# Performance work log

Hardware: AMD Instinct MI355X
Metric: run time of the kernel (lower is better)

Reference implementation:

```python
import jax, jax.numpy as jnp
import numpy as np

DIM = 512
HEADS = 8
D_HEAD = 64
INNER = HEADS * D_HEAD  # 512
CTX_DIM = 768
FF_INNER = 4 * DIM  # 2048
SCALE = D_HEAD ** -0.5
LN_EPS = 1e-5


def layer_norm(x, g, b):
    mu = jnp.mean(x, axis=-1, keepdims=True)
    var = jnp.var(x, axis=-1, keepdims=True)
    return (x - mu) * jax.lax.rsqrt(var + LN_EPS) * g + b


def attention(x, ctx, qw, kw, vw, ow, ob):
    B, N, _ = x.shape
    M = ctx.shape[1]
    q = (x @ qw).reshape(B, N, HEADS, D_HEAD).transpose(0, 2, 1, 3)
    k = (ctx @ kw).reshape(B, M, HEADS, D_HEAD).transpose(0, 2, 1, 3)
    v = (ctx @ vw).reshape(B, M, HEADS, D_HEAD).transpose(0, 2, 1, 3)
    sim = jnp.einsum('bhid,bhjd->bhij', q, k) * SCALE  # [B,H,N,M]
    attn = jax.nn.softmax(sim, axis=-1)
    out = jnp.einsum('bhij,bhjd->bhid', attn, v)
    out = out.transpose(0, 2, 1, 3).reshape(B, N, INNER)
    return out @ ow + ob


def setup_inputs() -> dict:
    key = jax.random.key(0)
    ks = jax.random.split(key, 20)
    r = lambda k, shp, s=0.02: jax.random.normal(k, shp, dtype=jnp.float32) * s
    return {
        'x': jax.random.normal(ks[0], (2, 4096, DIM), dtype=jnp.float32),
        'context': jax.random.normal(ks[1], (2, 256, CTX_DIM), dtype=jnp.float32),
        'q1_w': r(ks[2], (DIM, INNER)), 'k1_w': r(ks[3], (DIM, INNER)),
        'v1_w': r(ks[4], (DIM, INNER)), 'o1_w': r(ks[5], (INNER, DIM)),
        'o1_b': jnp.zeros((DIM,), jnp.float32),
        'q2_w': r(ks[6], (DIM, INNER)), 'k2_w': r(ks[7], (CTX_DIM, INNER)),
        'v2_w': r(ks[8], (CTX_DIM, INNER)), 'o2_w': r(ks[9], (INNER, DIM)),
        'o2_b': jnp.zeros((DIM,), jnp.float32),
        'ff_in_w': r(ks[10], (DIM, 2 * FF_INNER)), 'ff_in_b': jnp.zeros((2 * FF_INNER,), jnp.float32),
        'ff_out_w': r(ks[11], (FF_INNER, DIM)), 'ff_out_b': jnp.zeros((DIM,), jnp.float32),
        'ln1_g': jnp.ones((DIM,), jnp.float32), 'ln1_b': jnp.zeros((DIM,), jnp.float32),
        'ln2_g': jnp.ones((DIM,), jnp.float32), 'ln2_b': jnp.zeros((DIM,), jnp.float32),
        'ln3_g': jnp.ones((DIM,), jnp.float32), 'ln3_b': jnp.zeros((DIM,), jnp.float32),
    }


def reference(x, context, q1_w, k1_w, v1_w, o1_w, o1_b,
              q2_w, k2_w, v2_w, o2_w, o2_b,
              ff_in_w, ff_in_b, ff_out_w, ff_out_b,
              ln1_g, ln1_b, ln2_g, ln2_b, ln3_g, ln3_b):
    # self-attention + residual
    h = layer_norm(x, ln1_g, ln1_b)
    x = attention(h, h, q1_w, k1_w, v1_w, o1_w, o1_b) + x
    # cross-attention + residual
    h = layer_norm(x, ln2_g, ln2_b)
    x = attention(h, context, q2_w, k2_w, v2_w, o2_w, o2_b) + x
    # GEGLU feed-forward + residual (torch F.gelu is exact erf form)
    h = layer_norm(x, ln3_g, ln3_b)
    proj = h @ ff_in_w + ff_in_b
    val, gate = jnp.split(proj, 2, axis=-1)
    ff = (val * jax.nn.gelu(gate, approximate=False)) @ ff_out_w + ff_out_b
    return ff + x
```

## Files before the change

### kernel.cpp

```cpp
#include <hip/hip_runtime.h>
#include <hip/hip_bf16.h>
#include <cstdint>


typedef __bf16 bf16_t;
typedef __bf16 bf16x8 __attribute__((ext_vector_type(8)));
typedef float f32x4 __attribute__((ext_vector_type(4)));
typedef float f32x16 __attribute__((ext_vector_type(16)));

__device__ __forceinline__ bf16_t f2bf(float f) { return (bf16_t)f; }

__device__ __forceinline__ f32x4 mfma16(bf16x8 a, bf16x8 b, f32x4 c) {
  return __builtin_amdgcn_mfma_f32_16x16x32_bf16(a, b, c, 0, 0, 0);
}
__device__ __forceinline__ f32x16 mfma32(bf16x8 a, bf16x8 b, f32x16 c) {
  return __builtin_amdgcn_mfma_f32_32x32x16_bf16(a, b, c, 0, 0, 0);
}

__device__ __forceinline__ float gelu_exact(float x) {
  return 0.5f * x * (1.0f + erff(x * 0.70710678118654752f));
}

__device__ __forceinline__ void gload_lds16(const bf16_t* g, bf16_t* lds) {
  __builtin_amdgcn_global_load_lds(
      (const __attribute__((address_space(1))) unsigned int*)g,
      (__attribute__((address_space(3))) unsigned int*)lds, 16, 0, 0);
}

__global__ __launch_bounds__(256) void ln_kernel(const float* __restrict__ in,
                                                 const float* __restrict__ gw,
                                                 const float* __restrict__ bw,
                                                 bf16_t* __restrict__ out) {
  int w = threadIdx.x >> 6, l = threadIdx.x & 63;
  size_t row = (size_t)blockIdx.x * 4 + w;
  const float* p = in + row * 512 + l * 8;
  f32x4 va = *(const f32x4*)p;
  f32x4 vb = *(const f32x4*)(p + 4);
  float xs[8] = {va[0], va[1], va[2], va[3], vb[0], vb[1], vb[2], vb[3]};
  float s = 0.f;
#pragma unroll
  for (int j = 0; j < 8; j++) s += xs[j];
#pragma unroll
  for (int m = 1; m < 64; m <<= 1) s += __shfl_xor(s, m);
  float mu = s * (1.0f / 512.0f);
  float v = 0.f;
#pragma unroll
  for (int j = 0; j < 8; j++) { float d = xs[j] - mu; v += d * d; }
#pragma unroll
  for (int m = 1; m < 64; m <<= 1) v += __shfl_xor(v, m);
  float rstd = rsqrtf(v * (1.0f / 512.0f) + 1e-5f);
  f32x4 g0 = *(const f32x4*)(gw + l * 8);
  f32x4 g1 = *(const f32x4*)(gw + l * 8 + 4);
  f32x4 b0 = *(const f32x4*)(bw + l * 8);
  f32x4 b1 = *(const f32x4*)(bw + l * 8 + 4);
  bf16x8 o;
#pragma unroll
  for (int j = 0; j < 4; j++) o[j] = f2bf((xs[j] - mu) * rstd * g0[j] + b0[j]);
#pragma unroll
  for (int j = 0; j < 4; j++) o[4 + j] = f2bf((xs[4 + j] - mu) * rstd * g1[j] + b1[j]);
  *(bf16x8*)(out + row * 512 + l * 8) = o;
}

struct WJob {
  const float* W;
  bf16_t* Wt;
  int K;
  int N;
  float sc;
  int tile0;
};
struct WJobs {
  WJob j[10];
};

__global__ __launch_bounds__(256) void wtrans_all_kernel(WJobs jobs) {
  __shared__ float t[32][33];
  int bid = blockIdx.x;
  int i = 0;
#pragma unroll
  for (int q = 1; q < 10; q++)
    if (bid >= jobs.j[q].tile0) i = q;
  WJob jb = jobs.j[i];
  int tt = bid - jb.tile0;
  int ktiles = jb.K >> 5;
  int k0 = (tt % ktiles) * 32, n0 = (tt / ktiles) * 32;
#pragma unroll
  for (int s = 0; s < 4; s++) {
    int idx = threadIdx.x + s * 256;
    int kk = idx >> 5, nn = idx & 31;
    t[kk][nn] = jb.W[(size_t)(k0 + kk) * jb.N + n0 + nn];
  }
  __syncthreads();
#pragma unroll
  for (int s = 0; s < 4; s++) {
    int idx = threadIdx.x + s * 256;
    int nn = idx >> 5, kk = idx & 31;
    jb.Wt[(size_t)(n0 + nn) * jb.K + k0 + kk] = f2bf(t[kk][nn] * jb.sc);
  }
}

__global__ __launch_bounds__(256) void cvt_kernel(const float* __restrict__ in,
                                                  bf16_t* __restrict__ out) {
  int i = (blockIdx.x * 256 + threadIdx.x) * 4;
  f32x4 v = *(const f32x4*)(in + i);
  out[i + 0] = f2bf(v[0]);
  out[i + 1] = f2bf(v[1]);
  out[i + 2] = f2bf(v[2]);
  out[i + 3] = f2bf(v[3]);
}

template <int BM, int BN, int EPI>
__global__ __launch_bounds__(256) void gemm_kernel(
    const bf16_t* __restrict__ A, const bf16_t* __restrict__ Bt,
    const float* __restrict__ bias, const float* __restrict__ res,
    void* __restrict__ outp, int M, int N, int K, int gateOff, int ldo) {
  constexpr int WR = BM / 2;
  constexpr int WN = BN / 2;
  constexpr int MF = WR / 16;
  constexpr int NF = WN / 16;
  constexpr int ABLK = BM / 64;
  constexpr int BROWS = (EPI == 2) ? 2 * BN : BN;
  constexpr int BBLK = BROWS / 64;
  __shared__ bf16_t Al[2][2][BM][32];
  __shared__ bf16_t Bl[2][2][BROWS][32];

  int tid = threadIdx.x;
  int w = tid >> 6, l = tid & 63;
  int wr = w >> 1, wc = w & 1;
  int lg = l >> 4, lc = l & 15;

  int ntiles = gridDim.y;
  int lin = blockIdx.y * gridDim.x + blockIdx.x;
  int cpx = (gridDim.x * gridDim.y) >> 3;
  int v = (lin & 7) * cpx + (lin >> 3);
  int m0 = (v / ntiles) * BM, n0 = (v % ntiles) * BN;

  f32x4 acc[MF][NF] = {};
  f32x4 acc2[MF][NF] = {};

  int srow = tid >> 2, scol = (tid & 3) * 8;
  const bf16_t* aP[ABLK];
#pragma unroll
  for (int i = 0; i < ABLK; i++)
    aP[i] = A + (size_t)(m0 + i * 64 + srow) * K + scol;
  const bf16_t* bP[BBLK];
  if (EPI == 2) {
    bP[0] = Bt + (size_t)(n0 + srow) * K + scol;
    bP[1] = Bt + (size_t)(n0 + gateOff + srow) * K + scol;
  } else {
#pragma unroll
    for (int i = 0; i < BBLK; i++)
      bP[i] = Bt + (size_t)(n0 + i * 64 + srow) * K + scol;
  }

  auto STAGE = [&](int buf, int k0) {
#pragma unroll
    for (int kh = 0; kh < 2; kh++) {
#pragma unroll
      for (int i = 0; i < ABLK; i++)
        gload_lds16(aP[i] + k0 + kh * 32, &Al[buf][kh][i * 64 + w * 16][0]);
#pragma unroll
      for (int i = 0; i < BBLK; i++)
        gload_lds16(bP[i] + k0 + kh * 32, &Bl[buf][kh][i * 64 + w * 16][0]);
    }
  };

  int nk = K / 64;
  int cur = 0;
  STAGE(0, 0);
  __syncthreads();

  for (int t = 0; t < nk; ++t) {
    if (t + 1 < nk) STAGE(cur ^ 1, (t + 1) * 64);

#pragma unroll
    for (int kh = 0; kh < 2; kh++) {
      bf16x8 af[MF];
#pragma unroll
      for (int mi = 0; mi < MF; mi++)
        af[mi] = *(const bf16x8*)&Al[cur][kh][wr * WR + mi * 16 + lc][lg * 8];
      bf16x8 bfr[NF];
#pragma unroll
      for (int ni = 0; ni < NF; ni++)
        bfr[ni] = *(const bf16x8*)&Bl[cur][kh][wc * WN + ni * 16 + lc][lg * 8];
#pragma unroll
      for (int mi = 0; mi < MF; mi++)
#pragma unroll
        for (int ni = 0; ni < NF; ni++)
          acc[mi][ni] = mfma16(af[mi], bfr[ni], acc[mi][ni]);
      if (EPI == 2) {
        bf16x8 bg[NF];
#pragma unroll
        for (int ni = 0; ni < NF; ni++)
          bg[ni] =
              *(const bf16x8*)&Bl[cur][kh][BN + wc * WN + ni * 16 + lc][lg * 8];
#pragma unroll
        for (int mi = 0; mi < MF; mi++)
#pragma unroll
          for (int ni = 0; ni < NF; ni++)
            acc2[mi][ni] = mfma16(af[mi], bg[ni], acc2[mi][ni]);
      }
    }
    __syncthreads();
    cur ^= 1;
  }

#pragma unroll
  for (int mi = 0; mi < MF; mi++) {
#pragma unroll
    for (int ni = 0; ni < NF; ni++) {
#pragma unroll
      for (int r = 0; r < 4; r++) {
        int row = m0 + wr * WR + mi * 16 + lg * 4 + r;
        int col = n0 + wc * WN + ni * 16 + lc;
        float v2 = acc[mi][ni][r];
        if (EPI == 0) {
          ((bf16_t*)outp)[(size_t)row * ldo + col] = f2bf(v2);
        } else if (EPI == 3) {
          int cs = (col & ~15) | (lc & 3) | ((lc & 4) << 1) | ((lc & 8) >> 1);
          ((bf16_t*)outp)[(size_t)row * ldo + cs] = f2bf(v2);
        } else if (EPI == 1) {
          ((float*)outp)[(size_t)row * ldo + col] =
              v2 + bias[col] + res[(size_t)row * ldo + col];
        } else {
          float g = acc2[mi][ni][r] + bias[col + gateOff];
          float val = v2 + bias[col];
          ((bf16_t*)outp)[(size_t)row * ldo + col] = f2bf(val * gelu_exact(g));
        }
      }
    }
  }
}

__global__ __launch_bounds__(256) void cross_fused_kernel(
    const bf16_t* __restrict__ hb, const bf16_t* __restrict__ q2t,
    bf16_t* __restrict__ qkb, const bf16_t* __restrict__ ctxb,
    const bf16_t* __restrict__ k2t, bf16_t* __restrict__ kb,
    const bf16_t* __restrict__ v2t, bf16_t* __restrict__ vtg2) {
  constexpr int BM = 64, BN = 128;
  constexpr int WR = 32, WN = 64, MF = 2, NF = 4;
  __shared__ bf16_t Al[2][2][BM][32];
  __shared__ bf16_t Bl[2][2][BN][32];

  const bf16_t* A;
  const bf16_t* Bt;
  bf16_t* outp;
  int K, m0;
  bool perm = false;
  if (blockIdx.z == 0) {
    A = hb; Bt = q2t; outp = qkb; K = 512; m0 = blockIdx.x * BM;
  } else {
    int bx = blockIdx.x;
    if (bx >= 16) return;
    K = 768;
    if (bx < 8) {
      A = ctxb; Bt = k2t; outp = kb; m0 = bx * BM;
    } else {
      A = v2t; Bt = ctxb; outp = vtg2; perm = true; m0 = (bx - 8) * BM;
    }
  }
  const int ldo = 512;
  int n0 = blockIdx.y * BN;

  int tid = threadIdx.x;
  int w = tid >> 6, l = tid & 63;
  int wr = w >> 1, wc = w & 1;
  int lg = l >> 4, lc = l & 15;

  f32x4 acc[MF][NF] = {};

  int srow = tid >> 2, scol = (tid & 3) * 8;
  const bf16_t* aP0 = A + (size_t)(m0 + srow) * K + scol;
  const bf16_t* bP0 = Bt + (size_t)(n0 + srow) * K + scol;
  const bf16_t* bP1 = Bt + (size_t)(n0 + 64 + srow) * K + scol;

  auto STAGE = [&](int buf, int k0) {
#pragma unroll
    for (int kh = 0; kh < 2; kh++) {
      gload_lds16(aP0 + k0 + kh * 32, &Al[buf][kh][w * 16][0]);
      gload_lds16(bP0 + k0 + kh * 32, &Bl[buf][kh][w * 16][0]);
      gload_lds16(bP1 + k0 + kh * 32, &Bl[buf][kh][64 + w * 16][0]);
    }
  };

  int nk = K / 64;
  int cur = 0;
  STAGE(0, 0);
  __syncthreads();

  for (int t = 0; t < nk; ++t) {
    if (t + 1 < nk) STAGE(cur ^ 1, (t + 1) * 64);
#pragma unroll
    for (int kh = 0; kh < 2; kh++) {
      bf16x8 af[MF];
#pragma unroll
      for (int mi = 0; mi < MF; mi++)
        af[mi] = *(const bf16x8*)&Al[cur][kh][wr * WR + mi * 16 + lc][lg * 8];
      bf16x8 bfr[NF];
#pragma unroll
      for (int ni = 0; ni < NF; ni++)
        bfr[ni] = *(const bf16x8*)&Bl[cur][kh][wc * WN + ni * 16 + lc][lg * 8];
#pragma unroll
      for (int mi = 0; mi < MF; mi++)
#pragma unroll
        for (int ni = 0; ni < NF; ni++)
          acc[mi][ni] = mfma16(af[mi], bfr[ni], acc[mi][ni]);
    }
    __syncthreads();
    cur ^= 1;
  }

#pragma unroll
  for (int mi = 0; mi < MF; mi++) {
#pragma unroll
    for (int ni = 0; ni < NF; ni++) {
#pragma unroll
      for (int r = 0; r < 4; r++) {
        int row = m0 + wr * WR + mi * 16 + lg * 4 + r;
        int col = n0 + wc * WN + ni * 16 + lc;
        int cs = perm ? ((col & ~15) | (lc & 3) | ((lc & 4) << 1) |
                         ((lc & 8) >> 1))
                      : col;
        outp[(size_t)row * ldo + cs] = f2bf(acc[mi][ni][r]);
      }
    }
  }
}

__global__ __launch_bounds__(256) void attn_kernel(
    const bf16_t* __restrict__ Q, int ldq, const bf16_t* __restrict__ Kb,
    int ldk, const bf16_t* __restrict__ Vt, bf16_t* __restrict__ O, int Mkv) {
  __shared__ bf16_t Klds[2][64][72];
  __shared__ bf16_t Vlds[2][64][72];

  int lin = blockIdx.x;
  int xcd = lin & 7, slot = lin >> 3;
  int pair = 2 * xcd + (slot >> 5);
  int qt = slot & 31;
  int head = pair & 7, b = pair >> 3;

  int tid = threadIdx.x;
  int w = tid >> 6, l = tid & 63;
  int ql = l & 31, hi = l >> 5;
  int ldv = 2 * Mkv;

  size_t qrow = (size_t)b * 4096 + qt * 128 + w * 32 + ql;
  const bf16_t* qp = Q + qrow * ldq + head * 64 + hi * 8;
  bf16x8 qf[4];
#pragma unroll
  for (int dk = 0; dk < 4; dk++) qf[dk] = *(const bf16x8*)(qp + dk * 16);

  f32x16 o0 = {}, o1 = {};
  f32x16 zacc = {};
  float mrun = -1e30f;

  bf16x8 vones;
#pragma unroll
  for (int j = 0; j < 8; j++) vones[j] = f2bf(1.0f);

  int key0 = tid >> 2, dc0 = (tid & 3) * 16;
  const bf16_t* kp = Kb + ((size_t)b * Mkv + key0) * ldk + head * 64 + dc0;
  const bf16_t* vp = Vt + (size_t)(head * 64 + key0) * ldv + b * Mkv + dc0;

  int nt = Mkv / 64;

  bf16x8 kc0 = *(const bf16x8*)kp, kc1 = *(const bf16x8*)(kp + 8);
  bf16x8 vc0 = *(const bf16x8*)vp, vc1 = *(const bf16x8*)(vp + 8);
  *(bf16x8*)&Klds[0][key0][dc0] = kc0;
  *(bf16x8*)&Klds[0][key0][dc0 + 8] = kc1;
  *(bf16x8*)&Vlds[0][key0][dc0] = vc0;
  *(bf16x8*)&Vlds[0][key0][dc0 + 8] = vc1;
  if (nt > 1) {
    kp += (size_t)64 * ldk;
    vp += 64;
    kc0 = *(const bf16x8*)kp;
    kc1 = *(const bf16x8*)(kp + 8);
    vc0 = *(const bf16x8*)vp;
    vc1 = *(const bf16x8*)(vp + 8);
  }
  __syncthreads();

  for (int t = 0; t < nt; ++t) {
    int cur = t & 1;

    f32x16 s0 = {}, s1 = {};
    __builtin_amdgcn_s_setprio(1);
#pragma unroll
    for (int dk = 0; dk < 4; dk++) {
      bf16x8 a0 = *(const bf16x8*)&Klds[cur][ql][dk * 16 + hi * 8];
      bf16x8 a1 = *(const bf16x8*)&Klds[cur][32 + ql][dk * 16 + hi * 8];
      s0 = mfma32(a0, qf[dk], s0);
      s1 = mfma32(a1, qf[dk], s1);
    }
    __builtin_amdgcn_s_setprio(0);

    float tmax = s0[0];
#pragma unroll
    for (int r = 1; r < 16; r++) tmax = fmaxf(tmax, s0[r]);
#pragma unroll
    for (int r = 0; r < 16; r++) tmax = fmaxf(tmax, s1[r]);
    tmax = fmaxf(tmax, __shfl_xor(tmax, 32));

    if (!__all(tmax <= mrun + 8.0f)) {
      float mnew = fmaxf(mrun, tmax);
      float resc = __builtin_amdgcn_exp2f(mrun - mnew);
      mrun = mnew;
#pragma unroll
      for (int r = 0; r < 16; r++) {
        float f = __shfl(resc, (r & 3) + 8 * (r >> 2) + 4 * hi);
        o0[r] *= f;
        o1[r] *= f;
        zacc[r] *= f;
      }
    }

    bf16x8 pa[4];
#pragma unroll
    for (int m = 0; m < 4; m++) {
#pragma unroll
      for (int j = 0; j < 8; j++) {
        float sv = (m < 2) ? s0[(m & 1) * 8 + j] : s1[(m & 1) * 8 + j];
        pa[m][j] = f2bf(__builtin_amdgcn_exp2f(sv - mrun));
      }
    }

    __builtin_amdgcn_s_setprio(1);
#pragma unroll
    for (int m = 0; m < 4; m++) {
      zacc = mfma32(pa[m], vones, zacc);
      bf16x8 vb0 = *(const bf16x8*)&Vlds[cur][ql][m * 16 + hi * 8];
      bf16x8 vb1 = *(const bf16x8*)&Vlds[cur][32 + ql][m * 16 + hi * 8];
      o0 = mfma32(pa[m], vb0, o0);
      o1 = mfma32(pa[m], vb1, o1);
    }
    __builtin_amdgcn_s_setprio(0);

    if (t + 1 < nt) {
      *(bf16x8*)&Klds[cur ^ 1][key0][dc0] = kc0;
      *(bf16x8*)&Klds[cur ^ 1][key0][dc0 + 8] = kc1;
      *(bf16x8*)&Vlds[cur ^ 1][key0][dc0] = vc0;
      *(bf16x8*)&Vlds[cur ^ 1][key0][dc0 + 8] = vc1;
      if (t + 2 < nt) {
        kp += (size_t)64 * ldk;
        vp += 64;
        kc0 = *(const bf16x8*)kp;
        kc1 = *(const bf16x8*)(kp + 8);
        vc0 = *(const bf16x8*)vp;
        vc1 = *(const bf16x8*)(vp + 8);
      }
      __syncthreads();
    }
  }

  size_t ob = ((size_t)b * 4096 + qt * 128 + w * 32) * 512 + head * 64;
#pragma unroll
  for (int r = 0; r < 16; r++) {
    float inv = 1.0f / zacc[r];
    int q = (r & 3) + 8 * (r >> 2) + 4 * hi;
    O[ob + (size_t)q * 512 + ql] = f2bf(o0[r] * inv);
    O[ob + (size_t)q * 512 + 32 + ql] = f2bf(o1[r] * inv);
  }
}

extern "C" void kernel_launch(void* const* d_in, const int* in_sizes, int n_in,
                              void* d_out, int out_size, void* d_ws,
                              size_t ws_size, hipStream_t stream) {
  const float* x = (const float*)d_in[0];
  const float* ctx = (const float*)d_in[1];
  const float* q1_w = (const float*)d_in[2];
  const float* k1_w = (const float*)d_in[3];
  const float* v1_w = (const float*)d_in[4];
  const float* o1_w = (const float*)d_in[5];
  const float* o1_b = (const float*)d_in[6];
  const float* q2_w = (const float*)d_in[7];
  const float* k2_w = (const float*)d_in[8];
  const float* v2_w = (const float*)d_in[9];
  const float* o2_w = (const float*)d_in[10];
  const float* o2_b = (const float*)d_in[11];
  const float* ff_in_w = (const float*)d_in[12];
  const float* ff_in_b = (const float*)d_in[13];
  const float* ff_out_w = (const float*)d_in[14];
  const float* ff_out_b = (const float*)d_in[15];
  const float* ln1_g = (const float*)d_in[16];
  const float* ln1_b = (const float*)d_in[17];
  const float* ln2_g = (const float*)d_in[18];
  const float* ln2_b = (const float*)d_in[19];
  const float* ln3_g = (const float*)d_in[20];
  const float* ln3_b = (const float*)d_in[21];

  char* ws = (char*)d_ws;
  float* xr = (float*)(ws + 0);
  bf16_t* hb = (bf16_t*)(ws + 16777216);
  bf16_t* qkb = (bf16_t*)(ws + 25165824);
  bf16_t* ao = (bf16_t*)(ws + 41943040);
  bf16_t* ffmid = qkb;
  bf16_t* kb = (bf16_t*)(ws + 50331648);
  bf16_t* vtg2 = (bf16_t*)(ws + 50855936);
  bf16_t* ctxb = (bf16_t*)(ws + 51380224);
  bf16_t* wts = (bf16_t*)(ws + 58720256);
  bf16_t* vtg = (bf16_t*)(ws + 69730304);

  bf16_t* q1t = wts + 0;
  bf16_t* k1t = wts + 262144;
  bf16_t* v1t = wts + 524288;
  bf16_t* o1t = wts + 786432;
  bf16_t* q2t = wts + 1048576;
  bf16_t* k2t = wts + 1310720;
  bf16_t* v2t = wts + 1703936;
  bf16_t* o2t = wts + 2097152;
  bf16_t* ffint = wts + 2359296;
  bf16_t* ffoutt = wts + 4456448;

  const float QS = 0.125f * 1.44269504f;

  WJobs jobs;
  auto setj = [&](int i, const float* W, bf16_t* Wt, int K, int N, float sc,
                  int tile0) {
    jobs.j[i] = WJob{W, Wt, K, N, sc, tile0};
  };
  setj(0, q1_w, q1t, 512, 512, QS, 0);
  setj(1, k1_w, k1t, 512, 512, 1.0f, 256);
  setj(2, v1_w, v1t, 512, 512, 1.0f, 512);
  setj(3, o1_w, o1t, 512, 512, 1.0f, 768);
  setj(4, q2_w, q2t, 512, 512, QS, 1024);
  setj(5, k2_w, k2t, 768, 512, 1.0f, 1280);
  setj(6, v2_w, v2t, 768, 512, 1.0f, 1664);
  setj(7, o2_w, o2t, 512, 512, 1.0f, 2048);
  setj(8, ff_in_w, ffint, 512, 4096, 1.0f, 2304);
  setj(9, ff_out_w, ffoutt, 2048, 512, 1.0f, 4352);
  wtrans_all_kernel<<<5376, 256, 0, stream>>>(jobs);
  cvt_kernel<<<384, 256, 0, stream>>>(ctx, ctxb);

  ln_kernel<<<2048, 256, 0, stream>>>(x, ln1_g, ln1_b, hb);
  gemm_kernel<128, 128, 0><<<dim3(64, 8), 256, 0, stream>>>(
      hb, q1t, nullptr, nullptr, qkb, 8192, 1024, 512, 0, 1024);
  gemm_kernel<64, 128, 3><<<dim3(8, 64), 256, 0, stream>>>(
      v1t, hb, nullptr, nullptr, vtg, 512, 8192, 512, 0, 8192);
  attn_kernel<<<512, 256, 0, stream>>>(qkb, 1024, qkb + 512, 1024, vtg, ao,
                                       4096);
  gemm_kernel<64, 128, 1><<<dim3(128, 4), 256, 0, stream>>>(
      ao, o1t, o1_b, x, xr, 8192, 512, 512, 0, 512);

  ln_kernel<<<2048, 256, 0, stream>>>(xr, ln2_g, ln2_b, hb);
  cross_fused_kernel<<<dim3(128, 4, 2), 256, 0, stream>>>(
      hb, q2t, qkb, ctxb, k2t, kb, v2t, vtg2);
  attn_kernel<<<512, 256, 0, stream>>>(qkb, 512, kb, 512, vtg2, ao, 256);
  gemm_kernel<64, 128, 1><<<dim3(128, 4), 256, 0, stream>>>(
      ao, o2t, o2_b, xr, xr, 8192, 512, 512, 0, 512);

  ln_kernel<<<2048, 256, 0, stream>>>(xr, ln3_g, ln3_b, hb);
  gemm_kernel<128, 64, 2><<<dim3(64, 32), 256, 0, stream>>>(
      hb, ffint, ff_in_b, nullptr, ffmid, 8192, 2048, 512, 2048, 2048);
  gemm_kernel<64, 128, 1><<<dim3(128, 4), 256, 0, stream>>>(
      ffmid, ffoutt, ff_out_b, xr, (float*)d_out, 8192, 512, 2048, 0, 512);
}
```

Measured before the change: 282.7 us.

## Software-pipeline attention QK of next tile with softmax/PV of current tile

Restructures the attention inner loop into a two-stage software pipeline. The QK^T MFMAs for tile t+1 are issued before the softmax and PV of tile t, with the loop unrolled by two and alternating score registers. LDS buffers grow from 2 to 3 so a K/V tile stays readable while the next one is written. The goal is to overlap exp and softmax VALU work with matrix-core work. In exchange, register pressure rises from the extra score accumulators and LDS use grows, which may reduce occupancy.

```diff
diff --git a/kernel.cpp b/kernel.cpp
--- a/kernel.cpp
+++ b/kernel.cpp
@@ -330,8 +330,8 @@
 __global__ __launch_bounds__(256) void attn_kernel(
     const bf16_t* __restrict__ Q, int ldq, const bf16_t* __restrict__ Kb,
     int ldk, const bf16_t* __restrict__ Vt, bf16_t* __restrict__ O, int Mkv) {
-  __shared__ bf16_t Klds[2][64][72];
-  __shared__ bf16_t Vlds[2][64][72];
+  __shared__ bf16_t Klds[3][64][72];
+  __shared__ bf16_t Vlds[3][64][72];
 
   int lin = blockIdx.x;
   int xcd = lin & 7, slot = lin >> 3;
@@ -353,6 +353,7 @@
   f32x16 o0 = {}, o1 = {};
   f32x16 zacc = {};
   float mrun = -1e30f;
+  const f32x16 fzero = {};
 
   bf16x8 vones;
 #pragma unroll
@@ -362,38 +363,36 @@
   const bf16_t* kp = Kb + ((size_t)b * Mkv + key0) * ldk + head * 64 + dc0;
   const bf16_t* vp = Vt + (size_t)(head * 64 + key0) * ldv + b * Mkv + dc0;
 
-  int nt = Mkv / 64;
-
-  bf16x8 kc0 = *(const bf16x8*)kp, kc1 = *(const bf16x8*)(kp + 8);
-  bf16x8 vc0 = *(const bf16x8*)vp, vc1 = *(const bf16x8*)(vp + 8);
-  *(bf16x8*)&Klds[0][key0][dc0] = kc0;
-  *(bf16x8*)&Klds[0][key0][dc0 + 8] = kc1;
-  *(bf16x8*)&Vlds[0][key0][dc0] = vc0;
-  *(bf16x8*)&Vlds[0][key0][dc0 + 8] = vc1;
-  if (nt > 1) {
-    kp += (size_t)64 * ldk;
-    vp += 64;
+  bf16x8 kc0, kc1, vc0, vc1;
+
+  auto LOADCUR = [&]() {
     kc0 = *(const bf16x8*)kp;
     kc1 = *(const bf16x8*)(kp + 8);
     vc0 = *(const bf16x8*)vp;
     vc1 = *(const bf16x8*)(vp + 8);
-  }
-  __syncthreads();
-
-  for (int t = 0; t < nt; ++t) {
-    int cur = t & 1;
-
-    f32x16 s0 = {}, s1 = {};
+  };
+  auto ADVANCE = [&]() {
+    kp += (size_t)64 * ldk;
+    vp += 64;
+  };
+  auto WRITE = [&](int buf) {
+    *(bf16x8*)&Klds[buf][key0][dc0] = kc0;
+    *(bf16x8*)&Klds[buf][key0][dc0 + 8] = kc1;
+    *(bf16x8*)&Vlds[buf][key0][dc0] = vc0;
+    *(bf16x8*)&Vlds[buf][key0][dc0 + 8] = vc1;
+  };
+  auto QK = [&](int buf, f32x16& s0, f32x16& s1) {
     __builtin_amdgcn_s_setprio(1);
 #pragma unroll
     for (int dk = 0; dk < 4; dk++) {
-      bf16x8 a0 = *(const bf16x8*)&Klds[cur][ql][dk * 16 + hi * 8];
-      bf16x8 a1 = *(const bf16x8*)&Klds[cur][32 + ql][dk * 16 + hi * 8];
+      bf16x8 a0 = *(const bf16x8*)&Klds[buf][ql][dk * 16 + hi * 8];
+      bf16x8 a1 = *(const bf16x8*)&Klds[buf][32 + ql][dk * 16 + hi * 8];
       s0 = mfma32(a0, qf[dk], s0);
       s1 = mfma32(a1, qf[dk], s1);
     }
     __builtin_amdgcn_s_setprio(0);
-
+  };
+  auto SMPV = [&](int t, f32x16& s0, f32x16& s1) {
     float tmax = s0[0];
 #pragma unroll
     for (int r = 1; r < 16; r++) tmax = fmaxf(tmax, s0[r]);
@@ -424,32 +423,58 @@
       }
     }
 
+    int vb = t % 3;
     __builtin_amdgcn_s_setprio(1);
 #pragma unroll
     for (int m = 0; m < 4; m++) {
       zacc = mfma32(pa[m], vones, zacc);
-      bf16x8 vb0 = *(const bf16x8*)&Vlds[cur][ql][m * 16 + hi * 8];
-      bf16x8 vb1 = *(const bf16x8*)&Vlds[cur][32 + ql][m * 16 + hi * 8];
+      bf16x8 vb0 = *(const bf16x8*)&Vlds[vb][ql][m * 16 + hi * 8];
+      bf16x8 vb1 = *(const bf16x8*)&Vlds[vb][32 + ql][m * 16 + hi * 8];
       o0 = mfma32(pa[m], vb0, o0);
       o1 = mfma32(pa[m], vb1, o1);
     }
     __builtin_amdgcn_s_setprio(0);
-
+  };
+
+  int nt = Mkv / 64;
+
+  LOADCUR();
+  WRITE(0);
+  if (nt > 1) {
+    ADVANCE();
+    LOADCUR();
+  }
+  __syncthreads();
+
+  f32x16 sA0 = {}, sA1 = {};
+  QK(0, sA0, sA1);
+
+  for (int t = 0; t < nt; t += 2) {
+    f32x16 sB0 = {}, sB1 = {};
     if (t + 1 < nt) {
-      *(bf16x8*)&Klds[cur ^ 1][key0][dc0] = kc0;
-      *(bf16x8*)&Klds[cur ^ 1][key0][dc0 + 8] = kc1;
-      *(bf16x8*)&Vlds[cur ^ 1][key0][dc0] = vc0;
-      *(bf16x8*)&Vlds[cur ^ 1][key0][dc0 + 8] = vc1;
+      WRITE((t + 1) % 3);
       if (t + 2 < nt) {
-        kp += (size_t)64 * ldk;
-        vp += 64;
-        kc0 = *(const bf16x8*)kp;
-        kc1 = *(const bf16x8*)(kp + 8);
-        vc0 = *(const bf16x8*)vp;
-        vc1 = *(const bf16x8*)(vp + 8);
+        ADVANCE();
+        LOADCUR();
       }
       __syncthreads();
-    }
+      QK((t + 1) % 3, sB0, sB1);
+    }
+    SMPV(t, sA0, sA1);
+    if (t + 1 >= nt) break;
+
+    sA0 = fzero;
+    sA1 = fzero;
+    if (t + 2 < nt) {
+      WRITE((t + 2) % 3);
+      if (t + 3 < nt) {
+        ADVANCE();
+        LOADCUR();
+      }
+      __syncthreads();
+      QK((t + 2) % 3, sA0, sA1);
+    }
+    SMPV(t + 1, sB0, sB1);
   }
 
   size_t ob = ((size_t)b * 4096 + qt * 128 + w * 32) * 512 + head * 64;
```

Result: slower. 347.6 us (+22.9%).
